# Kernel tuning notes

Hardware: AMD Instinct MI355X
Metric: run time of the kernel (lower is better)

Reference implementation:

```python
import jax, jax.numpy as jnp
import numpy as np

INPUTDIM = 256
OUTDIM = 256
GRIDSIZE = 300
SCALE_BASE = 1.0
SCALE_FOURIER = 1.0
BATCH = 2048


def setup_inputs() -> dict:
    key = jax.random.key(0)
    k_x, k_bw, k_fc = jax.random.split(key, 3)
    x = jax.random.normal(k_x, (BATCH, INPUTDIM), dtype=jnp.float32)
    # HeUniform for base_weight: limit = sqrt(6 / fan_in)
    limit = np.sqrt(6.0 / INPUTDIM)
    base_weight = jax.random.uniform(
        k_bw, (INPUTDIM, OUTDIM), dtype=jnp.float32, minval=-limit, maxval=limit)
    stddev = 1.0 / (np.sqrt(INPUTDIM) * np.sqrt(GRIDSIZE))
    fouriercoeffs = (jax.random.normal(k_fc, (2, OUTDIM, INPUTDIM, GRIDSIZE), dtype=jnp.float32)
                     * jnp.float32(stddev))
    return {"x": x, "base_weight": base_weight, "fouriercoeffs": fouriercoeffs}


def reference(x, base_weight, fouriercoeffs):
    # Base path: silu(x @ W)
    base_output = jax.nn.silu(x @ base_weight)  # [B, J]
    # Fourier feature expansion: k = 1..gridsize
    k = jnp.arange(1, GRIDSIZE + 1, dtype=x.dtype)  # [K]
    theta = x[:, :, None] * k[None, None, :]        # [B, I, K]
    c = jnp.cos(theta)
    s = jnp.sin(theta)
    # einsum 'dbik,djik->bj' split into cos and sin parts
    fourier_output = (jnp.einsum('bik,jik->bj', c, fouriercoeffs[0])
                      + jnp.einsum('bik,jik->bj', s, fouriercoeffs[1]))
    return SCALE_BASE * base_output + SCALE_FOURIER * fourier_output
```

## Files before the change

### kernel.cpp

```cpp
#include <hip/hip_runtime.h>
#include <hip/hip_bf16.h>
#include <cstdint>

#define BATCH   2048
#define INDIM   256
#define OUTDIM  256
#define KGRID   300
#define NCHUNK  10

typedef __attribute__((ext_vector_type(4))) float f32x4;
typedef __attribute__((ext_vector_type(2))) float f32x2;
typedef __attribute__((ext_vector_type(8))) short bf16x8;

__device__ __forceinline__ uint32_t pack_bf16x2(float lo, float hi) {
    union { __hip_bfloat162 h; uint32_t u; } cv;
    cv.h = __float22bfloat162_rn(make_float2(lo, hi));
    return cv.u;
}

__device__ __forceinline__ f32x2 pk_fma_sub(f32x2 a, f32x2 b, f32x2 c) {
    f32x2 d;
    asm("v_pk_fma_f32 %0, %1, %2, %3 neg_lo:[0,0,1] neg_hi:[0,0,1]"
        : "=v"(d) : "v"(a), "v"(b), "v"(c));
    return d;
}

__device__ __forceinline__ void load_lds16(const void* g, void* l) {
    __builtin_amdgcn_global_load_lds(
        (const __attribute__((address_space(1))) void*)g,
        (__attribute__((address_space(3))) void*)l, 16, 0, 0);
}

#define PACKED_U4 ((size_t)INDIM * NCHUNK * OUTDIM * 8)
#define PACKED_BYTES (PACKED_U4 * 16)

__global__ __launch_bounds__(256) void pack_kernel(
    const float* __restrict__ fc, uint4* __restrict__ pk)
{
    size_t tidg = (size_t)blockIdx.x * 256 + threadIdx.x;
    int sub = tidg & 7;
    int j   = (tidg >> 3) & 255;
    int ich = (int)(tidg >> 11);
    int ch  = ich % NCHUNK;
    int i   = ich / NCHUNK;
    int kb  = ch * 32 + (sub ^ (j & 7)) * 4;
    if (kb > KGRID - 4) kb = KGRID - 4;
    const float* pc = fc + ((size_t)j * INDIM + i) * KGRID + kb;
    const float* ps = pc + (size_t)OUTDIM * INDIM * KGRID;
    float4 vc = *reinterpret_cast<const float4*>(pc);
    float4 vs = *reinterpret_cast<const float4*>(ps);
    uint4 wv;
    wv.x = pack_bf16x2(vc.x, vs.x);
    wv.y = pack_bf16x2(vc.y, vs.y);
    wv.z = pack_bf16x2(vc.z, vs.z);
    wv.w = pack_bf16x2(vc.w, vs.w);
    pk[tidg] = wv;
}

__global__ __launch_bounds__(256, 2) void fourier_dma_kernel(
    const float* __restrict__ x, const uint4* __restrict__ pk,
    float* __restrict__ part)
{
    __shared__ uint4 Abuf[128][8];
    __shared__ uint4 Bbuf[2][256][8];

    const int tid = threadIdx.x;
    const int flat = blockIdx.x + (blockIdx.z << 4);
    const int L  = (flat & 7) * 64 + (flat >> 3);
    const int b0 = (L & 15) * 128;
    const int z  = L >> 4;
    const int i0 = z * 8;

    const int lane = tid & 63, wave = tid >> 6;
    const int wm = wave >> 1, wn = wave & 1;
    const int lrow = lane & 15, lgrp = lane >> 4;
    const int grow = tid >> 1,  gh = tid & 1;
    const int q8 = wave * 8;

    f32x4 acc[2][4][4] = {};
    float thc, thn, c1v, s1v, t2v;

    thn = x[(size_t)(b0 + grow) * INDIM + i0];

    {
        const uint4* src = pk + (size_t)(i0 * NCHUNK) * 2048;
        char* dst = (char*)&Bbuf[0][0][0];
        #pragma unroll
        for (int q = 0; q < 8; ++q)
            load_lds16(src + (q8 + q) * 64 + lane, dst + (q8 + q) * 1024);
    }

    int il = 0, ch = 0;
    #pragma unroll 1
    for (int t = 0; t < 8 * NCHUNK; ++t) {
        if (ch == 0) {
            thc = thn;
            __sincosf(thc, &s1v, &c1v);
            t2v = 2.f * c1v;
            int iln = (il + 1 < 8) ? il + 1 : il;
            thn = x[(size_t)(b0 + grow) * INDIM + i0 + iln];
        }
        {
            int il2 = il, ch2 = ch + 1;
            if (ch2 == NCHUNK) { ch2 = 0; il2 = (il + 1 < 8) ? il + 1 : il; }
            const uint4* src = pk + (size_t)((i0 + il2) * NCHUNK + ch2) * 2048;
            char* dst = (char*)&Bbuf[(t + 1) & 1][0][0];
            #pragma unroll
            for (int q = 0; q < 8; ++q)
                load_lds16(src + (q8 + q) * 64 + lane, dst + (q8 + q) * 1024);
        }
        {
            const int k0 = ch * 32 + gh * 16;
            float ck, sk;
            __sincosf(thc * (float)(k0 + 1), &sk, &ck);
            float cp = __builtin_fmaf(ck, c1v,  sk * s1v);
            float sp = __builtin_fmaf(sk, c1v, -ck * s1v);
            f32x2 C; C.x = ck; C.y = sk;
            f32x2 P; P.x = cp; P.y = sp;
            f32x2 T2; T2.x = t2v; T2.y = t2v;
            const int swz = grow & 7;
            #pragma unroll
            for (int c = 0; c < 4; ++c) {
                uint32_t uu[4];
                #pragma unroll
                for (int qq = 0; qq < 4; ++qq) {
                    uu[qq] = pack_bf16x2(C.x, C.y);
                    f32x2 N = pk_fma_sub(T2, C, P);
                    P = C; C = N;
                }
                if (ch == NCHUNK - 1) {
                    #pragma unroll
                    for (int qq = 0; qq < 4; ++qq)
                        if (k0 + c * 4 + qq >= KGRID) uu[qq] = 0u;
                }
                Abuf[grow][(gh * 4 + c) ^ swz] =
                    make_uint4(uu[0], uu[1], uu[2], uu[3]);
            }
        }
        __syncthreads();
        __builtin_amdgcn_s_setprio(1);
        #pragma unroll
        for (int s = 0; s < 2; ++s) {
            bf16x8 afr[4];
            #pragma unroll
            for (int mf = 0; mf < 4; ++mf) {
                const int rowA = wm * 64 + mf * 16 + lrow;
                uint4 tv = Abuf[rowA][(s * 4 + lgrp) ^ (rowA & 7)];
                afr[mf] = *reinterpret_cast<bf16x8*>(&tv);
            }
            #pragma unroll
            for (int ns = 0; ns < 2; ++ns)
                #pragma unroll
                for (int nf = 0; nf < 4; ++nf) {
                    const int jl = wn * 128 + ns * 64 + nf * 16 + lrow;
                    uint4 tv = Bbuf[t & 1][jl][(s * 4 + lgrp) ^ (jl & 7)];
                    bf16x8 bfr = *reinterpret_cast<bf16x8*>(&tv);
                    #pragma unroll
                    for (int mf = 0; mf < 4; ++mf)
                        acc[ns][mf][nf] = __builtin_amdgcn_mfma_f32_16x16x32_bf16(
                            afr[mf], bfr, acc[ns][mf][nf], 0, 0, 0);
                }
        }
        __builtin_amdgcn_s_setprio(0);
        __syncthreads();
        if (++ch == NCHUNK) { ch = 0; ++il; }
    }

    float* pws = part + (size_t)z * BATCH * OUTDIM;
    #pragma unroll
    for (int ns = 0; ns < 2; ++ns)
        #pragma unroll
        for (int mf = 0; mf < 4; ++mf)
            #pragma unroll
            for (int nf = 0; nf < 4; ++nf)
                #pragma unroll
                for (int r = 0; r < 4; ++r) {
                    int b = b0 + wm * 64 + mf * 16 + lgrp * 4 + r;
                    int j = wn * 128 + ns * 64 + nf * 16 + lrow;
                    pws[(size_t)b * OUTDIM + j] = acc[ns][mf][nf][r];
                }
}

__global__ __launch_bounds__(256, 2) void fourier_kernel_fb(
    const float* __restrict__ x, const float* __restrict__ fc,
    float* __restrict__ ws, int ips)
{
    __shared__ uint4 Abuf[2][128][8];
    __shared__ uint4 Bbuf[128][8];

    const int tid  = threadIdx.x;
    const int b0   = blockIdx.x * 256;
    const int j0   = blockIdx.y * 128;
    const int i0   = blockIdx.z * ips;

    const int lane = tid & 63, wave = tid >> 6;
    const int wm   = wave >> 1, wn = wave & 1;
    const int lrow = lane & 15, lgrp = lane >> 4;
    const int grow = tid >> 1,  gh = tid & 1;

    f32x4 acc[2][4][4] = {};

    #pragma unroll 1
    for (int il = 0; il < ips; ++il) {
        const int i = i0 + il;
        float th[2], c1[2], s1[2], t2[2];
        th[0] = x[(size_t)(b0 + grow)       * INDIM + i];
        th[1] = x[(size_t)(b0 + 128 + grow) * INDIM + i];
        #pragma unroll
        for (int m = 0; m < 2; ++m) {
            __sincosf(th[m], &s1[m], &c1[m]);
            t2[m] = 2.f * c1[m];
        }
        #pragma unroll 1
        for (int ch = 0; ch < NCHUNK; ++ch) {
            #pragma unroll
            for (int r = 0; r < 4; ++r) {
                int flat = r * 256 + tid;
                int jl = flat >> 3, sub = flat & 7;
                int kb = ch * 32 + sub * 4;
                if (kb > KGRID - 4) kb = KGRID - 4;
                const float* pc = fc + ((size_t)(j0 + jl) * INDIM + i) * KGRID + kb;
                const float* ps = pc + (size_t)OUTDIM * INDIM * KGRID;
                float4 vc = *reinterpret_cast<const float4*>(pc);
                float4 vs = *reinterpret_cast<const float4*>(ps);
                uint4 wv;
                wv.x = pack_bf16x2(vc.x, vs.x);
                wv.y = pack_bf16x2(vc.y, vs.y);
                wv.z = pack_bf16x2(vc.z, vs.z);
                wv.w = pack_bf16x2(vc.w, vs.w);
                Bbuf[jl][sub ^ (jl & 7)] = wv;
            }
            #pragma unroll
            for (int m = 0; m < 2; ++m) {
                const int k0 = ch * 32 + gh * 16;
                float ck, sk;
                __sincosf(th[m] * (float)(k0 + 1), &sk, &ck);
                float cp = __builtin_fmaf(ck, c1[m],  sk * s1[m]);
                float sp = __builtin_fmaf(sk, c1[m], -ck * s1[m]);
                const int swz = grow & 7;
                #pragma unroll
                for (int c = 0; c < 4; ++c) {
                    uint32_t uu[4];
                    #pragma unroll
                    for (int qq = 0; qq < 4; ++qq) {
                        const int kidx = k0 + c * 4 + qq;
                        float cc = (kidx < KGRID) ? ck : 0.f;
                        float ss = (kidx < KGRID) ? sk : 0.f;
                        uu[qq] = pack_bf16x2(cc, ss);
                        float cn = __builtin_fmaf(t2[m], ck, -cp);
                        float sn = __builtin_fmaf(t2[m], sk, -sp);
                        cp = ck; sp = sk; ck = cn; sk = sn;
                    }
                    Abuf[m][grow][(gh * 4 + c) ^ swz] =
                        make_uint4(uu[0], uu[1], uu[2], uu[3]);
                }
            }
            __syncthreads();
            #pragma unroll
            for (int s = 0; s < 2; ++s) {
                bf16x8 bfr[4];
                #pragma unroll
                for (int nf = 0; nf < 4; ++nf) {
                    const int jl = wn * 64 + nf * 16 + lrow;
                    uint4 tv = Bbuf[jl][(s * 4 + lgrp) ^ (jl & 7)];
                    bfr[nf] = *reinterpret_cast<bf16x8*>(&tv);
                }
                #pragma unroll
                for (int m = 0; m < 2; ++m) {
                    #pragma unroll
                    for (int mf = 0; mf < 4; ++mf) {
                        const int rowA = wm * 64 + mf * 16 + lrow;
                        uint4 tv = Abuf[m][rowA][(s * 4 + lgrp) ^ (rowA & 7)];
                        bf16x8 af = *reinterpret_cast<bf16x8*>(&tv);
                        #pragma unroll
                        for (int nf = 0; nf < 4; ++nf)
                            acc[m][mf][nf] = __builtin_amdgcn_mfma_f32_16x16x32_bf16(
                                af, bfr[nf], acc[m][mf][nf], 0, 0, 0);
                    }
                }
            }
            __syncthreads();
        }
    }

    float* pws = ws + (size_t)blockIdx.z * BATCH * OUTDIM;
    #pragma unroll
    for (int m = 0; m < 2; ++m)
        #pragma unroll
        for (int mf = 0; mf < 4; ++mf)
            #pragma unroll
            for (int nf = 0; nf < 4; ++nf)
                #pragma unroll
                for (int r = 0; r < 4; ++r) {
                    int b = b0 + m * 128 + wm * 64 + mf * 16 + lgrp * 4 + r;
                    int j = j0 + wn * 64 + nf * 16 + lrow;
                    pws[(size_t)b * OUTDIM + j] = acc[m][mf][nf][r];
                }
}

__global__ __launch_bounds__(256) void combine_kernel(
    const float* __restrict__ x, const float* __restrict__ w,
    const float* __restrict__ part, float* __restrict__ out, int nsplit)
{
    __shared__ float Xs[64][16];
    __shared__ float Wt[16][68];

    const int tid = threadIdx.x;
    const int b0 = blockIdx.x * 64;
    const int j0 = blockIdx.y * 64;
    const int tx = tid & 15, ty = tid >> 4;

    float acc[4][4] = {};

    for (int kb = 0; kb < INDIM; kb += 16) {
        {
            int m = tid >> 2, kq = (tid & 3) * 4;
            float4 v = *reinterpret_cast<const float4*>(
                &x[(size_t)(b0 + m) * INDIM + kb + kq]);
            Xs[m][kq+0] = v.x; Xs[m][kq+1] = v.y; Xs[m][kq+2] = v.z; Xs[m][kq+3] = v.w;
        }
        {
            int kr = tid >> 4, jc = (tid & 15) * 4;
            float4 v = *reinterpret_cast<const float4*>(
                &w[(size_t)(kb + kr) * OUTDIM + j0 + jc]);
            Wt[kr][jc+0] = v.x; Wt[kr][jc+1] = v.y; Wt[kr][jc+2] = v.z; Wt[kr][jc+3] = v.w;
        }
        __syncthreads();
        #pragma unroll
        for (int kk = 0; kk < 16; ++kk) {
            float a[4], b[4];
            #pragma unroll
            for (int q = 0; q < 4; ++q) { a[q] = Xs[ty*4+q][kk]; b[q] = Wt[kk][tx*4+q]; }
            #pragma unroll
            for (int q = 0; q < 4; ++q)
                #pragma unroll
                for (int p = 0; p < 4; ++p)
                    acc[q][p] = __builtin_fmaf(a[q], b[p], acc[q][p]);
        }
        __syncthreads();
    }

    float psum[4][4] = {};
    for (int s = 0; s < nsplit; ++s) {
        const float* base = part + (size_t)s * BATCH * OUTDIM;
        #pragma unroll
        for (int q = 0; q < 4; ++q) {
            float4 pv = *reinterpret_cast<const float4*>(
                &base[(size_t)(b0 + ty*4 + q) * OUTDIM + j0 + tx*4]);
            psum[q][0] += pv.x; psum[q][1] += pv.y;
            psum[q][2] += pv.z; psum[q][3] += pv.w;
        }
    }

    #pragma unroll
    for (int q = 0; q < 4; ++q)
        #pragma unroll
        for (int p = 0; p < 4; ++p) {
            float v = acc[q][p];
            float sv = v / (1.f + __expf(-v));
            out[(size_t)(b0 + ty*4 + q) * OUTDIM + (j0 + tx*4 + p)] =
                sv + psum[q][p];
        }
}

extern "C" void kernel_launch(void* const* d_in, const int* in_sizes, int n_in,
                              void* d_out, int out_size, void* d_ws, size_t ws_size,
                              hipStream_t stream) {
    const float* x  = (const float*)d_in[0];
    const float* bw = (const float*)d_in[1];
    const float* fc = (const float*)d_in[2];
    float* out = (float*)d_out;

    const size_t per = (size_t)BATCH * OUTDIM * sizeof(float);

    if (ws_size >= PACKED_BYTES + 32 * per) {
        uint4* pk   = (uint4*)d_ws;
        float* part = (float*)((char*)d_ws + PACKED_BYTES);
        pack_kernel<<<(int)(PACKED_U4 / 256), 256, 0, stream>>>(fc, pk);
        fourier_dma_kernel<<<dim3(16, 1, 32), 256, 0, stream>>>(x, pk, part);
        combine_kernel<<<dim3(BATCH / 64, OUTDIM / 64), 256, 0, stream>>>(
            x, bw, part, out, 32);
    } else {
        float* part = (float*)d_ws;
        int S = 32;
        while (S > 1 && (size_t)S * per > ws_size) S >>= 1;
        const int ips = INDIM / S;
        fourier_kernel_fb<<<dim3(BATCH / 256, OUTDIM / 128, S), 256, 0, stream>>>(
            x, fc, part, ips);
        combine_kernel<<<dim3(BATCH / 64, OUTDIM / 64), 256, 0, stream>>>(
            x, bw, part, out, S);
    }
}
```

Baseline: 226.3 us.

## Generate Fourier A-fragments in registers instead of staging through LDS

Each wave now computes its own bf16 cos/sin MFMA A-fragments directly in registers, using angle-addition recurrences with precomputed sin/cos of 16θ and 32θ per row. This removes the LDS Abuf, its writes and reads, and the bank traffic that came with them. Because of how the 4x2 wave tile is split, the two waves sharing rows each generate those fragments, so generation work is duplicated. Register pressure rises from the extra per-row state, and the longer recurrence chains may cost accuracy. The MFMA loop is also reordered so all B fragments are loaded before the multiplies.

```diff
diff --git a/kernel.cpp b/kernel.cpp
--- a/kernel.cpp
+++ b/kernel.cpp
@@ -29,6 +29,28 @@
     __builtin_amdgcn_global_load_lds(
         (const __attribute__((address_space(1))) void*)g,
         (__attribute__((address_space(3))) void*)l, 16, 0, 0);
+}
+
+__device__ __forceinline__ bf16x8 zero_frag() {
+    union { uint32_t u[4]; bf16x8 v; } z = {{0u, 0u, 0u, 0u}};
+    return z.v;
+}
+
+__device__ __forceinline__ bf16x8 gen_frag(float ck, float sk,
+                                           float c1, float s1, float t2) {
+    float cp = __builtin_fmaf(ck, c1,  sk * s1);
+    float sp = __builtin_fmaf(sk, c1, -ck * s1);
+    f32x2 C; C.x = ck; C.y = sk;
+    f32x2 P; P.x = cp; P.y = sp;
+    f32x2 T2; T2.x = t2; T2.y = t2;
+    union { uint32_t u[4]; bf16x8 v; } r;
+    #pragma unroll
+    for (int q = 0; q < 4; ++q) {
+        r.u[q] = pack_bf16x2(C.x, C.y);
+        f32x2 N = pk_fma_sub(T2, C, P);
+        P = C; C = N;
+    }
+    return r.v;
 }
 
 #define PACKED_U4 ((size_t)INDIM * NCHUNK * OUTDIM * 8)
@@ -61,7 +83,6 @@
     const float* __restrict__ x, const uint4* __restrict__ pk,
     float* __restrict__ part)
 {
-    __shared__ uint4 Abuf[128][8];
     __shared__ uint4 Bbuf[2][256][8];
 
     const int tid = threadIdx.x;
@@ -74,13 +95,19 @@
     const int lane = tid & 63, wave = tid >> 6;
     const int wm = wave >> 1, wn = wave & 1;
     const int lrow = lane & 15, lgrp = lane >> 4;
-    const int grow = tid >> 1,  gh = tid & 1;
     const int q8 = wave * 8;
 
     f32x4 acc[2][4][4] = {};
-    float thc, thn, c1v, s1v, t2v;
-
-    thn = x[(size_t)(b0 + grow) * INDIM + i0];
+
+    float thn[4];
+    float c1[4], s1[4], t2[4];
+    float c16[4], s16[4];
+    float c32[4], s32[4];
+    float cS[4], sS[4];
+
+    #pragma unroll
+    for (int mf = 0; mf < 4; ++mf)
+        thn[mf] = x[(size_t)(b0 + wm * 64 + mf * 16 + lrow) * INDIM + i0];
 
     {
         const uint4* src = pk + (size_t)(i0 * NCHUNK) * 2048;
@@ -93,13 +120,6 @@
     int il = 0, ch = 0;
     #pragma unroll 1
     for (int t = 0; t < 8 * NCHUNK; ++t) {
-        if (ch == 0) {
-            thc = thn;
-            __sincosf(thc, &s1v, &c1v);
-            t2v = 2.f * c1v;
-            int iln = (il + 1 < 8) ? il + 1 : il;
-            thn = x[(size_t)(b0 + grow) * INDIM + i0 + iln];
-        }
         {
             int il2 = il, ch2 = ch + 1;
             if (ch2 == NCHUNK) { ch2 = 0; il2 = (il + 1 < 8) ? il + 1 : il; }
@@ -109,57 +129,64 @@
             for (int q = 0; q < 8; ++q)
                 load_lds16(src + (q8 + q) * 64 + lane, dst + (q8 + q) * 1024);
         }
-        {
-            const int k0 = ch * 32 + gh * 16;
-            float ck, sk;
-            __sincosf(thc * (float)(k0 + 1), &sk, &ck);
-            float cp = __builtin_fmaf(ck, c1v,  sk * s1v);
-            float sp = __builtin_fmaf(sk, c1v, -ck * s1v);
-            f32x2 C; C.x = ck; C.y = sk;
-            f32x2 P; P.x = cp; P.y = sp;
-            f32x2 T2; T2.x = t2v; T2.y = t2v;
-            const int swz = grow & 7;
-            #pragma unroll
-            for (int c = 0; c < 4; ++c) {
-                uint32_t uu[4];
-                #pragma unroll
-                for (int qq = 0; qq < 4; ++qq) {
-                    uu[qq] = pack_bf16x2(C.x, C.y);
-                    f32x2 N = pk_fma_sub(T2, C, P);
-                    P = C; C = N;
-                }
-                if (ch == NCHUNK - 1) {
-                    #pragma unroll
-                    for (int qq = 0; qq < 4; ++qq)
-                        if (k0 + c * 4 + qq >= KGRID) uu[qq] = 0u;
-                }
-                Abuf[grow][(gh * 4 + c) ^ swz] =
-                    make_uint4(uu[0], uu[1], uu[2], uu[3]);
+        if (ch == 0) {
+            const float flg = (float)(lgrp * 4);
+            #pragma unroll
+            for (int mf = 0; mf < 4; ++mf) {
+                float th = thn[mf];
+                __sincosf(th, &s1[mf], &c1[mf]);
+                t2[mf] = 2.f * c1[mf];
+                __sincosf(16.f * th, &s16[mf], &c16[mf]);
+                c32[mf] = __builtin_fmaf(2.f * c16[mf], c16[mf], -1.f);
+                s32[mf] = 2.f * s16[mf] * c16[mf];
+                float a0 = __builtin_fmaf(flg, th, th);
+                __sincosf(a0, &sS[mf], &cS[mf]);
+            }
+            int iln = (il + 1 < 8) ? il + 1 : il;
+            #pragma unroll
+            for (int mf = 0; mf < 4; ++mf)
+                thn[mf] = x[(size_t)(b0 + wm * 64 + mf * 16 + lrow) * INDIM
+                            + i0 + iln];
+        }
+        bf16x8 af[2][4];
+        #pragma unroll
+        for (int mf = 0; mf < 4; ++mf) {
+            af[0][mf] = gen_frag(cS[mf], sS[mf], c1[mf], s1[mf], t2[mf]);
+            float ck = __builtin_fmaf(cS[mf], c16[mf], -sS[mf] * s16[mf]);
+            float sk = __builtin_fmaf(sS[mf], c16[mf],  cS[mf] * s16[mf]);
+            af[1][mf] = gen_frag(ck, sk, c1[mf], s1[mf], t2[mf]);
+            float cn = __builtin_fmaf(cS[mf], c32[mf], -sS[mf] * s32[mf]);
+            float sn = __builtin_fmaf(sS[mf], c32[mf],  cS[mf] * s32[mf]);
+            cS[mf] = cn; sS[mf] = sn;
+        }
+        if (ch == NCHUNK - 1) {
+            #pragma unroll
+            for (int mf = 0; mf < 4; ++mf) {
+                af[0][mf] = (lgrp == 3) ? zero_frag() : af[0][mf];
+                af[1][mf] = zero_frag();
             }
         }
         __syncthreads();
         __builtin_amdgcn_s_setprio(1);
         #pragma unroll
         for (int s = 0; s < 2; ++s) {
-            bf16x8 afr[4];
-            #pragma unroll
-            for (int mf = 0; mf < 4; ++mf) {
-                const int rowA = wm * 64 + mf * 16 + lrow;
-                uint4 tv = Abuf[rowA][(s * 4 + lgrp) ^ (rowA & 7)];
-                afr[mf] = *reinterpret_cast<bf16x8*>(&tv);
-            }
+            bf16x8 bfr[2][4];
             #pragma unroll
             for (int ns = 0; ns < 2; ++ns)
                 #pragma unroll
                 for (int nf = 0; nf < 4; ++nf) {
                     const int jl = wn * 128 + ns * 64 + nf * 16 + lrow;
                     uint4 tv = Bbuf[t & 1][jl][(s * 4 + lgrp) ^ (jl & 7)];
-                    bf16x8 bfr = *reinterpret_cast<bf16x8*>(&tv);
+                    bfr[ns][nf] = *reinterpret_cast<bf16x8*>(&tv);
+                }
+            #pragma unroll
+            for (int mf = 0; mf < 4; ++mf)
+                #pragma unroll
+                for (int ns = 0; ns < 2; ++ns)
                     #pragma unroll
-                    for (int mf = 0; mf < 4; ++mf)
+                    for (int nf = 0; nf < 4; ++nf)
                         acc[ns][mf][nf] = __builtin_amdgcn_mfma_f32_16x16x32_bf16(
-                            afr[mf], bfr, acc[ns][mf][nf], 0, 0, 0);
-                }
+                            af[s][mf], bfr[ns][nf], acc[ns][mf][nf], 0, 0, 0);
         }
         __builtin_amdgcn_s_setprio(0);
         __syncthreads();
```

New measurement: 415.3 us. 83.5% more time.
